# Kernel optimization log

Hardware: AMD Instinct MI355X
Metric: run time of the kernel (lower is better)

The kernel has to match this reference:

```python
import jax, jax.numpy as jnp
import numpy as np

B, T, S, D, L, V = 32, 64, 128, 512, 2, 32000
DSRC = 2 * D  # bidirectional encoder
PAD = 1


def setup_inputs() -> dict:
    key = jax.random.key(0)
    ks = jax.random.split(key, 16)
    sc = 0.05
    embed = jax.random.normal(ks[5], (V, D), jnp.float32) * sc
    embed = embed.at[PAD].set(0.0)  # padding_idx row is zero
    return {
        "prev_tgt_tokens": jax.random.randint(ks[0], (B, T), 0, V),
        "encoder_out": jax.random.normal(ks[1], (B, S, DSRC), jnp.float32),
        "hiddens": jax.random.normal(ks[2], (L, B, D), jnp.float32) * sc,
        "cells": jax.random.normal(ks[3], (L, B, D), jnp.float32) * sc,
        "src_mask": jax.random.randint(ks[4], (B, S), 0, 2).astype(bool),
        "embed": embed,
        "W_ih": jax.random.normal(ks[6], (L, 4 * D, D), jnp.float32) * sc,
        "W_hh": jax.random.normal(ks[7], (L, 4 * D, D), jnp.float32) * sc,
        "b_ih": jnp.zeros((L, 4 * D), jnp.float32),
        "b_hh": jnp.zeros((L, 4 * D), jnp.float32),
        "W_in": jax.random.normal(ks[8], (DSRC, D), jnp.float32) * sc,   # input_proj: d_tgt -> d_src
        "b_in": jnp.zeros((DSRC,), jnp.float32),
        "W_out": jax.random.normal(ks[9], (D, DSRC + D), jnp.float32) * sc,  # out_proj
        "b_out": jnp.zeros((D,), jnp.float32),
    }


def reference(prev_tgt_tokens, encoder_out, hiddens, cells, src_mask,
              embed, W_ih, W_hh, b_ih, b_hh, W_in, b_in, W_out, b_out):
    n_layers, _, d_model = hiddens.shape
    tgt_len = prev_tgt_tokens.shape[1]
    tgt_embed = embed[prev_tgt_tokens]          # [B, T, D]
    xs = jnp.swapaxes(tgt_embed, 0, 1)          # [T, B, D]

    def lstm_cell(x, h, c, l):
        gates = x @ W_ih[l].T + b_ih[l] + h @ W_hh[l].T + b_hh[l]  # [B, 4D]
        i, f, g, o = jnp.split(gates, 4, axis=-1)
        c2 = jax.nn.sigmoid(f) * c + jax.nn.sigmoid(i) * jnp.tanh(g)
        h2 = jax.nn.sigmoid(o) * jnp.tanh(c2)
        return h2, c2

    def step(h_carry, y_t):
        s = y_t
        new_h = []
        for l in range(n_layers):
            h2, c2 = lstm_cell(s, h_carry[l], cells[l], l)
            # Faithful to source bug: `prev_hiddens[l], prev_hiddens[l] = (hidden, cell)`
            # stores the NEW CELL into the hidden slot; prev_cells never updated.
            new_h.append(c2)
            s = h2
        # attention
        xq = s @ W_in.T + b_in                              # [B, DSRC]
        e = jnp.einsum('bsd,bd->bs', encoder_out, xq)       # [B, S]
        e = jnp.where(src_mask, -1e9, e)
        attn = jax.nn.softmax(e, axis=-1)
        ctx = jnp.einsum('bs,bsd->bd', attn, encoder_out)   # [B, DSRC]
        out_t = jnp.tanh(jnp.concatenate([ctx, s], axis=-1) @ W_out.T + b_out)
        return jnp.stack(new_h), out_t

    _, outs = jax.lax.scan(step, hiddens, xs)   # outs: [T, B, D]
    # faithful to torch.cat(outs, dim=0).view(-1, tgt_len, d_model)
    return outs.reshape(-1, d_model).reshape(-1, tgt_len, d_model)
```

## Files before the change

### kernel.cpp

```cpp
#include <hip/hip_runtime.h>
#include <math.h>

typedef unsigned short u16;
typedef __attribute__((ext_vector_type(4))) float f4;
typedef __attribute__((ext_vector_type(8))) unsigned short us8;
typedef __attribute__((ext_vector_type(8))) short bfrag;
typedef __attribute__((ext_vector_type(4))) float f32x4;

#define BB 32
#define TT 64
#define DD 512
#define G4_ 2048

__device__ __forceinline__ float sigf(float x) { return 1.0f / (1.0f + expf(-x)); }
__device__ __forceinline__ float bf2f(u16 u) {
    union { unsigned int i; float f; } v; v.i = ((unsigned int)u) << 16; return v.f;
}
__device__ __forceinline__ u16 f2bf(float f) {
    union { float f; unsigned int i; } v; v.f = f;
    unsigned int r = v.i + 0x7fffu + ((v.i >> 16) & 1u);
    return (u16)(r >> 16);
}

__global__ void k_flag(const unsigned char* __restrict__ m, int* __restrict__ flag) {
    int tid = threadIdx.x;
    int badbyte = 0, nonz_off = 0, evenu16_nz = 0;
    for (int i = tid * 16; i < tid * 16 + 16; i++) {
        unsigned char c = m[i];
        if (c > 1) badbyte = 1;
        if ((i & 3) != 0 && c != 0) nonz_off = 1;
    }
    const u16* mu = (const u16*)m;
    for (int i = tid * 8; i < tid * 8 + 8; i++) {
        if ((i & 1) == 0 && mu[i] != 0) evenu16_nz = 1;
    }
    __shared__ int s_bad, s_noff, s_env;
    if (tid == 0) { s_bad = 0; s_noff = 0; s_env = 0; }
    __syncthreads();
    if (badbyte) atomicOr(&s_bad, 1);
    if (nonz_off) atomicOr(&s_noff, 1);
    if (evenu16_nz) atomicOr(&s_env, 1);
    __syncthreads();
    if (tid == 0) {
        int f;
        if (s_bad) f = s_env ? 2 : 3;
        else       f = s_noff ? 0 : 1;
        *flag = f;
    }
}

__global__ void __launch_bounds__(256) k_init2(const float* __restrict__ hid,
                                               u16* __restrict__ h0s,
                                               u16* __restrict__ h1s) {
    int i = blockIdx.x * 256 + threadIdx.x;
    u16 v0 = f2bf(hid[i]), v1 = f2bf(hid[16384 + i]);
    h0s[i] = v0; h0s[16384 + i] = v0;
    h1s[i] = v1; h1s[16384 + i] = v1;
}

__global__ void __launch_bounds__(256) k_packIn(const float* __restrict__ Win,
                                                u16* __restrict__ Wp) {
    int g = blockIdx.x * 256 + threadIdx.x;
    int lane = g & 63, grp = g >> 6;
    int j16 = grp >> 4, ks = grp & 15;
    const float* src = &Win[((size_t)(j16 * 16 + (lane & 15))) * 512 + ks * 32 + (lane >> 4) * 8];
    u16* dst = &Wp[(size_t)g * 8];
    f4 v0 = *(const f4*)&src[0];
    f4 v1 = *(const f4*)&src[4];
    dst[0] = f2bf(v0[0]); dst[1] = f2bf(v0[1]); dst[2] = f2bf(v0[2]); dst[3] = f2bf(v0[3]);
    dst[4] = f2bf(v1[0]); dst[5] = f2bf(v1[1]); dst[6] = f2bf(v1[2]); dst[7] = f2bf(v1[3]);
}

__global__ void __launch_bounds__(256) k_packOut(const float* __restrict__ Wout,
                                                 u16* __restrict__ Wp) {
    int g = blockIdx.x * 256 + threadIdx.x;
    int lane = g & 63, grp = g >> 6;
    int j16 = grp / 48, ks = grp % 48;
    const float* src = &Wout[((size_t)(j16 * 16 + (lane & 15))) * 1536 + ks * 32 + (lane >> 4) * 8];
    u16* dst = &Wp[(size_t)g * 8];
    f4 v0 = *(const f4*)&src[0];
    f4 v1 = *(const f4*)&src[4];
    dst[0] = f2bf(v0[0]); dst[1] = f2bf(v0[1]); dst[2] = f2bf(v0[2]); dst[3] = f2bf(v0[3]);
    dst[4] = f2bf(v1[0]); dst[5] = f2bf(v1[1]); dst[6] = f2bf(v1[2]); dst[7] = f2bf(v1[3]);
}

__global__ void __launch_bounds__(256) k_packA(const float* __restrict__ Wih0,
                                               u16* __restrict__ Wp) {
    int g = blockIdx.x * 256 + threadIdx.x;
    int lane = g & 63, grp = g >> 6;
    int j16 = grp >> 4, ks = grp & 15;
    const float* src = &Wih0[((size_t)(j16 * 16 + (lane & 15))) * 512 + ks * 32 + (lane >> 4) * 8];
    u16* dst = &Wp[(size_t)g * 8];
    f4 v0 = *(const f4*)&src[0];
    f4 v1 = *(const f4*)&src[4];
    dst[0] = f2bf(v0[0]); dst[1] = f2bf(v0[1]); dst[2] = f2bf(v0[2]); dst[3] = f2bf(v0[3]);
    dst[4] = f2bf(v1[0]); dst[5] = f2bf(v1[1]); dst[6] = f2bf(v1[2]); dst[7] = f2bf(v1[3]);
}

__global__ void __launch_bounds__(256) k_packPh(const float* __restrict__ Wih,
                                                const float* __restrict__ Whh,
                                                u16* __restrict__ php) {
    int gidx = blockIdx.x * 256 + threadIdx.x;
    int m = gidx >> 17;
    int rem = gidx & 131071;
    int lane = rem & 63;
    int q = rem >> 6;
    int ks = q & 15, T = q >> 4;
    int g = T >> 5, d16 = T & 31;
    int j = g * 512 + d16 * 16 + (lane & 15);
    int kcol = ks * 32 + (lane >> 4) * 8;
    const float* src = (m == 0) ? Whh
                     : (m == 1) ? (Wih + 1048576)
                                : (Whh + 1048576);
    const float* sp = &src[(size_t)j * 512 + kcol];
    u16* dst = &php[((size_t)m << 20) + (size_t)rem * 8];
    f4 v0 = *(const f4*)&sp[0];
    f4 v1 = *(const f4*)&sp[4];
    dst[0] = f2bf(v0[0]); dst[1] = f2bf(v0[1]); dst[2] = f2bf(v0[2]); dst[3] = f2bf(v0[3]);
    dst[4] = f2bf(v1[0]); dst[5] = f2bf(v1[1]); dst[6] = f2bf(v1[2]); dst[7] = f2bf(v1[3]);
}

__global__ void __launch_bounds__(256) k_gih0_mfma(const int* __restrict__ tokens,
                                                   const float* __restrict__ embed,
                                                   const u16* __restrict__ Wp,
                                                   const float* __restrict__ bih,
                                                   const float* __restrict__ bhh,
                                                   float* __restrict__ gih0p) {
    const int tid = threadIdx.x;
    const int lane = tid & 63, w = tid >> 6;
    const int t = blockIdx.y;
    const int jw = blockIdx.x * 256 + w * 64;
    __shared__ u16 xs[32][520];
    __shared__ int toks[32];
    if (tid < 32) toks[tid] = tokens[tid * TT + t];
    __syncthreads();
    for (int i = tid; i < 32 * 128; i += 256) {
        int b = i >> 7, k4 = i & 127;
        f4 v = *(const f4*)&embed[(size_t)toks[b] * 512 + k4 * 4];
        u16* dst = &xs[b][k4 * 4];
        dst[0] = f2bf(v[0]); dst[1] = f2bf(v[1]); dst[2] = f2bf(v[2]); dst[3] = f2bf(v[3]);
    }
    __syncthreads();

    const int l15 = lane & 15, l4 = lane >> 4;
    f32x4 acc[2][4];
#pragma unroll
    for (int mi = 0; mi < 2; mi++)
#pragma unroll
        for (int ni = 0; ni < 4; ni++) acc[mi][ni] = (f32x4){0.f, 0.f, 0.f, 0.f};

    for (int ks = 0; ks < 16; ks++) {
        bfrag a0 = *(const bfrag*)&xs[l15][ks * 32 + l4 * 8];
        bfrag a1 = *(const bfrag*)&xs[16 + l15][ks * 32 + l4 * 8];
#pragma unroll
        for (int ni = 0; ni < 4; ni++) {
            int j16 = (jw + ni * 16) >> 4;
            bfrag bf = *(const bfrag*)&Wp[(((size_t)j16 * 16 + ks) * 64 + lane) * 8];
            acc[0][ni] = __builtin_amdgcn_mfma_f32_16x16x32_bf16(a0, bf, acc[0][ni], 0, 0, 0);
            acc[1][ni] = __builtin_amdgcn_mfma_f32_16x16x32_bf16(a1, bf, acc[1][ni], 0, 0, 0);
        }
    }

#pragma unroll
    for (int ni = 0; ni < 4; ni++) {
        int j16 = (jw >> 4) + ni;
        int g = j16 >> 5, d16 = j16 & 31;
        int j = j16 * 16 + l15;
        float bv = bih[j] + bhh[j];
#pragma unroll
        for (int mi = 0; mi < 2; mi++) {
            f32x4 sv = acc[mi][ni];
            sv[0] += bv; sv[1] += bv; sv[2] += bv; sv[3] += bv;
            *(f32x4*)&gih0p[(((((size_t)t * 32 + d16) * 4 + g) * 2 + mi) * 64 + lane) * 4] = sv;
        }
    }
}

__global__ void __launch_bounds__(256) k_phaseM(
    const int k,
    const float* __restrict__ gih0p,
    const u16* __restrict__ whh0p,
    const u16* __restrict__ wih1p,
    const u16* __restrict__ whh1p,
    const float* __restrict__ bih1,
    const float* __restrict__ bhh1,
    const float* __restrict__ cells,
    const u16* __restrict__ h0r, u16* __restrict__ h0w,
    const u16* __restrict__ h20r, u16* __restrict__ h20w,
    const u16* __restrict__ h1r, u16* __restrict__ h1w,
    u16* __restrict__ H2)
{
    const int tid = threadIdx.x;
    const int lane = tid & 63, w = tid >> 6;
    const int l15 = lane & 15, l4 = lane >> 4;
    __shared__ u16 xsA[32][520];
    __shared__ u16 xsB[32][520];

    if (blockIdx.x < 16) {
        if (k >= 64) return;
        const int wid = blockIdx.x * 4 + w;
        const int d16 = wid >> 1, mi = wid & 1;
        const int d = d16 * 16 + l15;
        f32x4 acc[4];
#pragma unroll
        for (int g = 0; g < 4; g++)
            acc[g] = *(const f32x4*)&gih0p[(((((size_t)k * 32 + d16) * 4 + g) * 2 + mi) * 64 + lane) * 4];
        for (int i = tid; i < 2048; i += 256) {
            int b = i >> 6, k8 = i & 63;
            *(us8*)&xsA[b][k8 * 8] = *(const us8*)&h0r[b * 512 + k8 * 8];
        }
        __syncthreads();
        const int arow = mi * 16 + l15;
        for (int ks = 0; ks < 16; ks++) {
            bfrag a = *(const bfrag*)&xsA[arow][ks * 32 + l4 * 8];
#pragma unroll
            for (int g = 0; g < 4; g++) {
                int T = g * 32 + d16;
                bfrag bf = *(const bfrag*)&whh0p[(((size_t)T * 16 + ks) * 64 + lane) * 8];
                acc[g] = __builtin_amdgcn_mfma_f32_16x16x32_bf16(a, bf, acc[g], 0, 0, 0);
            }
        }
#pragma unroll
        for (int r = 0; r < 4; r++) {
            int b = mi * 16 + l4 * 4 + r;
            float gi = acc[0][r];
            float gf = acc[1][r];
            float gg = acc[2][r];
            float go = acc[3][r];
            float cell = cells[b * 512 + d];
            float c2 = sigf(gf) * cell + sigf(gi) * tanhf(gg);
            float h2 = sigf(go) * tanhf(c2);
            h0w[b * 512 + d] = f2bf(c2);
            h20w[b * 512 + d] = f2bf(h2);
        }
    } else {
        if (k < 1) return;
        for (int i = tid; i < 2048; i += 256) {
            int b = i >> 6, k8 = i & 63;
            *(us8*)&xsA[b][k8 * 8] = *(const us8*)&h20r[b * 512 + k8 * 8];
            *(us8*)&xsB[b][k8 * 8] = *(const us8*)&h1r[b * 512 + k8 * 8];
        }
        __syncthreads();
        const int wid = (blockIdx.x - 16) * 4 + w;
        const int d16 = wid >> 1, mi = wid & 1;
        const int d = d16 * 16 + l15;
        const int arow = mi * 16 + l15;
        f32x4 acc[4];
#pragma unroll
        for (int g = 0; g < 4; g++) acc[g] = (f32x4){0.f, 0.f, 0.f, 0.f};
        for (int ks = 0; ks < 16; ks++) {
            bfrag a = *(const bfrag*)&xsA[arow][ks * 32 + l4 * 8];
#pragma unroll
            for (int g = 0; g < 4; g++) {
                int T = g * 32 + d16;
                bfrag bf = *(const bfrag*)&wih1p[(((size_t)T * 16 + ks) * 64 + lane) * 8];
                acc[g] = __builtin_amdgcn_mfma_f32_16x16x32_bf16(a, bf, acc[g], 0, 0, 0);
            }
        }
        for (int ks = 0; ks < 16; ks++) {
            bfrag a = *(const bfrag*)&xsB[arow][ks * 32 + l4 * 8];
#pragma unroll
            for (int g = 0; g < 4; g++) {
                int T = g * 32 + d16;
                bfrag bf = *(const bfrag*)&whh1p[(((size_t)T * 16 + ks) * 64 + lane) * 8];
                acc[g] = __builtin_amdgcn_mfma_f32_16x16x32_bf16(a, bf, acc[g], 0, 0, 0);
            }
        }
        float bb0 = bih1[0 * 512 + d] + bhh1[0 * 512 + d];
        float bb1v = bih1[1 * 512 + d] + bhh1[1 * 512 + d];
        float bb2 = bih1[2 * 512 + d] + bhh1[2 * 512 + d];
        float bb3 = bih1[3 * 512 + d] + bhh1[3 * 512 + d];
#pragma unroll
        for (int r = 0; r < 4; r++) {
            int b = mi * 16 + l4 * 4 + r;
            float gi = acc[0][r] + bb0;
            float gf = acc[1][r] + bb1v;
            float gg = acc[2][r] + bb2;
            float go = acc[3][r] + bb3;
            float cell = cells[16384 + b * 512 + d];
            float c2 = sigf(gf) * cell + sigf(gi) * tanhf(gg);
            float h2 = sigf(go) * tanhf(c2);
            h1w[b * 512 + d] = f2bf(c2);
            H2[(size_t)(k - 1) * 16384 + b * 512 + d] = f2bf(h2);
        }
    }
}

__global__ void __launch_bounds__(256) k_x_mfma(const u16* __restrict__ H2,
                                                const u16* __restrict__ Wpin,
                                                const float* __restrict__ bin,
                                                float* __restrict__ XQ) {
    const int tid = threadIdx.x;
    const int lane = tid & 63, w = tid >> 6;
    const int t = blockIdx.y;
    const int jw = blockIdx.x * 256 + w * 64;
    __shared__ u16 xs[32][520];
    for (int i = tid; i < 2048; i += 256) {
        int b = i >> 6, k8 = i & 63;
        *(us8*)&xs[b][k8 * 8] = *(const us8*)&H2[(size_t)t * 16384 + b * 512 + k8 * 8];
    }
    __syncthreads();
    const int l15 = lane & 15, l4 = lane >> 4;
    f32x4 acc[2][4];
#pragma unroll
    for (int mi = 0; mi < 2; mi++)
#pragma unroll
        for (int ni = 0; ni < 4; ni++) acc[mi][ni] = (f32x4){0.f, 0.f, 0.f, 0.f};
    for (int ks = 0; ks < 16; ks++) {
        bfrag a0 = *(const bfrag*)&xs[l15][ks * 32 + l4 * 8];
        bfrag a1 = *(const bfrag*)&xs[16 + l15][ks * 32 + l4 * 8];
#pragma unroll
        for (int ni = 0; ni < 4; ni++) {
            int j16 = (jw + ni * 16) >> 4;
            bfrag bf = *(const bfrag*)&Wpin[(((size_t)j16 * 16 + ks) * 64 + lane) * 8];
            acc[0][ni] = __builtin_amdgcn_mfma_f32_16x16x32_bf16(a0, bf, acc[0][ni], 0, 0, 0);
            acc[1][ni] = __builtin_amdgcn_mfma_f32_16x16x32_bf16(a1, bf, acc[1][ni], 0, 0, 0);
        }
    }
#pragma unroll
    for (int ni = 0; ni < 4; ni++) {
        int j = jw + ni * 16 + l15;
        float bv = bin[j];
#pragma unroll
        for (int mi = 0; mi < 2; mi++) {
#pragma unroll
            for (int r = 0; r < 4; r++) {
                int b = mi * 16 + l4 * 4 + r;
                XQ[((size_t)(t * 32 + b)) * 1024 + j] = acc[mi][ni][r] + bv;
            }
        }
    }
}

__global__ void __launch_bounds__(256) k_out_mfma(const float* __restrict__ CTX,
                                                  const u16* __restrict__ H2,
                                                  const u16* __restrict__ Wpout,
                                                  const float* __restrict__ bout,
                                                  float* __restrict__ out) {
    const int tid = threadIdx.x;
    const int lane = tid & 63, w = tid >> 6;
    const int t = blockIdx.y;
    const int jw = blockIdx.x * 256 + w * 64;
    __shared__ u16 xs[32][520];
    const int l15 = lane & 15, l4 = lane >> 4;
    f32x4 acc[2][4];
#pragma unroll
    for (int mi = 0; mi < 2; mi++)
#pragma unroll
        for (int ni = 0; ni < 4; ni++) acc[mi][ni] = (f32x4){0.f, 0.f, 0.f, 0.f};
    for (int c = 0; c < 3; c++) {
        if (c) __syncthreads();
        if (c < 2) {
            for (int i = tid; i < 32 * 128; i += 256) {
                int b = i >> 7, k4 = i & 127;
                f4 v = *(const f4*)&CTX[((size_t)(t * 32 + b)) * 1024 + c * 512 + k4 * 4];
                u16* dst = &xs[b][k4 * 4];
                dst[0] = f2bf(v[0]); dst[1] = f2bf(v[1]); dst[2] = f2bf(v[2]); dst[3] = f2bf(v[3]);
            }
        } else {
            for (int i = tid; i < 2048; i += 256) {
                int b = i >> 6, k8 = i & 63;
                *(us8*)&xs[b][k8 * 8] = *(const us8*)&H2[(size_t)t * 16384 + b * 512 + k8 * 8];
            }
        }
        __syncthreads();
        for (int ks = 0; ks < 16; ks++) {
            bfrag a0 = *(const bfrag*)&xs[l15][ks * 32 + l4 * 8];
            bfrag a1 = *(const bfrag*)&xs[16 + l15][ks * 32 + l4 * 8];
#pragma unroll
            for (int ni = 0; ni < 4; ni++) {
                int j16 = (jw + ni * 16) >> 4;
                bfrag bf = *(const bfrag*)&Wpout[(((size_t)j16 * 48 + c * 16 + ks) * 64 + lane) * 8];
                acc[0][ni] = __builtin_amdgcn_mfma_f32_16x16x32_bf16(a0, bf, acc[0][ni], 0, 0, 0);
                acc[1][ni] = __builtin_amdgcn_mfma_f32_16x16x32_bf16(a1, bf, acc[1][ni], 0, 0, 0);
            }
        }
    }
#pragma unroll
    for (int ni = 0; ni < 4; ni++) {
        int j = jw + ni * 16 + l15;
        float bv = bout[j];
#pragma unroll
        for (int mi = 0; mi < 2; mi++) {
#pragma unroll
            for (int r = 0; r < 4; r++) {
                int b = mi * 16 + l4 * 4 + r;
                out[((size_t)(t * 32 + b)) * 512 + j] = tanhf(acc[mi][ni][r] + bv);
            }
        }
    }
}

__global__ void __launch_bounds__(256) k_att4(const float* __restrict__ XQ,
                                              const float* __restrict__ enc,
                                              const unsigned char* __restrict__ mask,
                                              const int* __restrict__ flag,
                                              float* __restrict__ CTX) {
    const int tid = threadIdx.x;
    const int b = blockIdx.x, t0 = blockIdx.y * 4;
    __shared__ float xq[4][1024];
    __shared__ float ered[4][256];
    __shared__ float attn[4][128];
    __shared__ float red2[4][8];
#pragma unroll
    for (int tg = 0; tg < 4; tg++) {
        f4 v = *(const f4*)&XQ[((size_t)((t0 + tg) * 32 + b)) * 1024 + tid * 4];
        float* dst = &xq[tg][tid * 4];
        dst[0] = v[0]; dst[1] = v[1]; dst[2] = v[2]; dst[3] = v[3];
    }
    __syncthreads();
    const int s = tid >> 1, hh = tid & 1;
    float p[4] = {0.f, 0.f, 0.f, 0.f};
    const float* erow = enc + ((size_t)(b * 128 + s)) * 1024 + hh * 512;
    for (int k4 = 0; k4 < 128; k4++) {
        f4 u = *(const f4*)&erow[k4 * 4];
#pragma unroll
        for (int kk = 0; kk < 4; kk++) {
#pragma unroll
            for (int tg = 0; tg < 4; tg++)
                p[tg] += u[kk] * xq[tg][hh * 512 + k4 * 4 + kk];
        }
    }
#pragma unroll
    for (int tg = 0; tg < 4; tg++) ered[tg][tid] = p[tg];
    __syncthreads();
    bool msk = false;
    if (tid < 128) {
        int f = *flag;
        if (f == 0)      msk = mask[b * 128 + tid] != 0;
        else if (f == 1) msk = ((const int*)mask)[b * 128 + tid] != 0;
        else if (f == 2) msk = ((const u16*)mask)[b * 128 + tid] != 0;
        else             msk = ((const unsigned int*)mask)[b * 128 + tid] != 0;
    }
    const int wave = tid >> 6;
    float e[4];
#pragma unroll
    for (int tg = 0; tg < 4; tg++) {
        e[tg] = -INFINITY;
        if (tid < 128) {
            e[tg] = ered[tg][2 * tid] + ered[tg][2 * tid + 1];
            if (msk) e[tg] = -1e9f;
        }
        float v = e[tg];
#pragma unroll
        for (int off = 32; off >= 1; off >>= 1) v = fmaxf(v, __shfl_xor(v, off));
        if ((tid & 63) == 0) red2[tg][wave] = v;
    }
    __syncthreads();
#pragma unroll
    for (int tg = 0; tg < 4; tg++) {
        float mx = fmaxf(fmaxf(red2[tg][0], red2[tg][1]), fmaxf(red2[tg][2], red2[tg][3]));
        float pp = (tid < 128) ? expf(e[tg] - mx) : 0.f;
        float su = pp;
#pragma unroll
        for (int off = 32; off >= 1; off >>= 1) su += __shfl_xor(su, off);
        if ((tid & 63) == 0) red2[tg][4 + wave] = su;
        __syncthreads();
        float S = (red2[tg][4] + red2[tg][5]) + (red2[tg][6] + red2[tg][7]);
        if (tid < 128) attn[tg][tid] = pp / S;
        __syncthreads();
    }
    float c0[4] = {0, 0, 0, 0}, c1[4] = {0, 0, 0, 0};
    float c2v[4] = {0, 0, 0, 0}, c3[4] = {0, 0, 0, 0};
    const float* eb = enc + ((size_t)b * 128) * 1024 + tid * 4;
    for (int s2 = 0; s2 < 128; s2++) {
        f4 u = *(const f4*)&eb[(size_t)s2 * 1024];
#pragma unroll
        for (int tg = 0; tg < 4; tg++) {
            float a = attn[tg][s2];
            c0[tg] += a * u[0]; c1[tg] += a * u[1]; c2v[tg] += a * u[2]; c3[tg] += a * u[3];
        }
    }
#pragma unroll
    for (int tg = 0; tg < 4; tg++) {
        float* crow = CTX + ((size_t)((t0 + tg) * 32 + b)) * 1024 + tid * 4;
        crow[0] = c0[tg]; crow[1] = c1[tg]; crow[2] = c2v[tg]; crow[3] = c3[tg];
    }
}

extern "C" void kernel_launch(void* const* d_in, const int* in_sizes, int n_in,
                              void* d_out, int out_size, void* d_ws, size_t ws_size,
                              hipStream_t stream) {
    const int* tokens   = (const int*)d_in[0];
    const float* enc    = (const float*)d_in[1];
    const float* hidden = (const float*)d_in[2];
    const float* cells  = (const float*)d_in[3];
    const unsigned char* mask = (const unsigned char*)d_in[4];
    const float* embed  = (const float*)d_in[5];
    const float* W_ih   = (const float*)d_in[6];
    const float* W_hh   = (const float*)d_in[7];
    const float* b_ih   = (const float*)d_in[8];
    const float* b_hh   = (const float*)d_in[9];
    const float* W_in   = (const float*)d_in[10];
    const float* b_in   = (const float*)d_in[11];
    const float* W_out  = (const float*)d_in[12];
    const float* b_out  = (const float*)d_in[13];
    float* out = (float*)d_out;

    float* ws = (float*)d_ws;
    float* gih0p = ws;
    u16*   h0s  = (u16*)(ws + 4194304);
    u16*   h20s = (u16*)(ws + 4210688);
    u16*   h1s  = (u16*)(ws + 4227072);
    u16*   H2   = (u16*)(ws + 4243456);
    u16*   php  = (u16*)(ws + 4767744);
    u16*   whh0p = php;
    u16*   wih1p = php + 1048576;
    u16*   whh1p = php + 2097152;
    u16*   wpin  = (u16*)(ws + 6340608);
    u16*   wpout = (u16*)(ws + 6602752);
    u16*   wih0p = (u16*)(ws + 6995968);
    int*   flag  = (int*)(ws + 7520256);
    float* XQ   = ws;
    float* CTX  = ws + 2097152;

    const float* bih1 = b_ih + G4_;
    const float* bhh1 = b_hh + G4_;

    k_flag<<<1, 256, 0, stream>>>(mask, flag);
    k_init2<<<64, 256, 0, stream>>>(hidden, h0s, h1s);
    k_packIn<<<256, 256, 0, stream>>>(W_in, wpin);
    k_packOut<<<384, 256, 0, stream>>>(W_out, wpout);
    k_packA<<<512, 256, 0, stream>>>(W_ih, wih0p);
    k_packPh<<<1536, 256, 0, stream>>>(W_ih, W_hh, php);
    k_gih0_mfma<<<dim3(8, 64), 256, 0, stream>>>(tokens, embed, wih0p, b_ih, b_hh, gih0p);

    for (int k = 0; k <= 64; k++) {
        const int r = k & 1, w = r ^ 1;
        k_phaseM<<<32, 256, 0, stream>>>(k, gih0p, whh0p, wih1p, whh1p, bih1, bhh1, cells,
                                         h0s + r * 16384, h0s + w * 16384,
                                         h20s + r * 16384, h20s + w * 16384,
                                         h1s + r * 16384, h1s + w * 16384, H2);
    }

    k_x_mfma<<<dim3(4, 64), 256, 0, stream>>>(H2, wpin, b_in, XQ);
    k_att4<<<dim3(32, 16), 256, 0, stream>>>(XQ, enc, mask, flag, CTX);
    k_out_mfma<<<dim3(2, 64), 256, 0, stream>>>(CTX, H2, wpout, b_out, out);
}
```

Before: 676.4 us.

## Split recurrent step K-reduction across wave pairs and double the block count

Each output tile of the per-timestep LSTM kernel is now computed by two waves that each handle half of the K dimension (layer 0) or one of the two matmuls (layer 1). The partial sums are combined through shared memory before the gate nonlinearities. Grid size doubles from 32 to 64 blocks, which spreads the latency-bound sequential step over more CUs. The cost is an extra __syncthreads, shared-memory reduction traffic, and each block restaging the full h vectors.

```diff
diff --git a/kernel.cpp b/kernel.cpp
--- a/kernel.cpp
+++ b/kernel.cpp
@@ -193,25 +193,32 @@
     const int tid = threadIdx.x;
     const int lane = tid & 63, w = tid >> 6;
     const int l15 = lane & 15, l4 = lane >> 4;
+    const int unitL = w >> 1, sub = w & 1;
     __shared__ u16 xsA[32][520];
     __shared__ u16 xsB[32][520];
-
-    if (blockIdx.x < 16) {
+    __shared__ float red[2][4][64][4];
+
+    if (blockIdx.x < 32) {
         if (k >= 64) return;
-        const int wid = blockIdx.x * 4 + w;
-        const int d16 = wid >> 1, mi = wid & 1;
+        const int d16mi = blockIdx.x * 2 + unitL;
+        const int d16 = d16mi >> 1, mi = d16mi & 1;
         const int d = d16 * 16 + l15;
         f32x4 acc[4];
 #pragma unroll
-        for (int g = 0; g < 4; g++)
-            acc[g] = *(const f32x4*)&gih0p[(((((size_t)k * 32 + d16) * 4 + g) * 2 + mi) * 64 + lane) * 4];
+        for (int g = 0; g < 4; g++) {
+            if (sub == 0)
+                acc[g] = *(const f32x4*)&gih0p[(((((size_t)k * 32 + d16) * 4 + g) * 2 + mi) * 64 + lane) * 4];
+            else
+                acc[g] = (f32x4){0.f, 0.f, 0.f, 0.f};
+        }
         for (int i = tid; i < 2048; i += 256) {
             int b = i >> 6, k8 = i & 63;
             *(us8*)&xsA[b][k8 * 8] = *(const us8*)&h0r[b * 512 + k8 * 8];
         }
         __syncthreads();
         const int arow = mi * 16 + l15;
-        for (int ks = 0; ks < 16; ks++) {
+        const int ks0 = sub * 8;
+        for (int ks = ks0; ks < ks0 + 8; ks++) {
             bfrag a = *(const bfrag*)&xsA[arow][ks * 32 + l4 * 8];
 #pragma unroll
             for (int g = 0; g < 4; g++) {
@@ -220,18 +227,31 @@
                 acc[g] = __builtin_amdgcn_mfma_f32_16x16x32_bf16(a, bf, acc[g], 0, 0, 0);
             }
         }
-#pragma unroll
-        for (int r = 0; r < 4; r++) {
-            int b = mi * 16 + l4 * 4 + r;
-            float gi = acc[0][r];
-            float gf = acc[1][r];
-            float gg = acc[2][r];
-            float go = acc[3][r];
-            float cell = cells[b * 512 + d];
-            float c2 = sigf(gf) * cell + sigf(gi) * tanhf(gg);
-            float h2 = sigf(go) * tanhf(c2);
-            h0w[b * 512 + d] = f2bf(c2);
-            h20w[b * 512 + d] = f2bf(h2);
+        if (sub == 1) {
+#pragma unroll
+            for (int g = 0; g < 4; g++)
+                *(f32x4*)&red[unitL][g][lane][0] = acc[g];
+        }
+        __syncthreads();
+        if (sub == 0) {
+#pragma unroll
+            for (int g = 0; g < 4; g++) {
+                f32x4 pv = *(const f32x4*)&red[unitL][g][lane][0];
+                acc[g][0] += pv[0]; acc[g][1] += pv[1]; acc[g][2] += pv[2]; acc[g][3] += pv[3];
+            }
+#pragma unroll
+            for (int r = 0; r < 4; r++) {
+                int b = mi * 16 + l4 * 4 + r;
+                float gi = acc[0][r];
+                float gf = acc[1][r];
+                float gg = acc[2][r];
+                float go = acc[3][r];
+                float cell = cells[b * 512 + d];
+                float c2 = sigf(gf) * cell + sigf(gi) * tanhf(gg);
+                float h2 = sigf(go) * tanhf(c2);
+                h0w[b * 512 + d] = f2bf(c2);
+                h20w[b * 512 + d] = f2bf(h2);
+            }
         }
     } else {
         if (k < 1) return;
@@ -241,47 +261,53 @@
             *(us8*)&xsB[b][k8 * 8] = *(const us8*)&h1r[b * 512 + k8 * 8];
         }
         __syncthreads();
-        const int wid = (blockIdx.x - 16) * 4 + w;
-        const int d16 = wid >> 1, mi = wid & 1;
+        const int d16mi = (blockIdx.x - 32) * 2 + unitL;
+        const int d16 = d16mi >> 1, mi = d16mi & 1;
         const int d = d16 * 16 + l15;
         const int arow = mi * 16 + l15;
+        const u16 (* __restrict__ xsrc)[520] = sub ? xsB : xsA;
+        const u16* wsrc = sub ? whh1p : wih1p;
         f32x4 acc[4];
 #pragma unroll
         for (int g = 0; g < 4; g++) acc[g] = (f32x4){0.f, 0.f, 0.f, 0.f};
         for (int ks = 0; ks < 16; ks++) {
-            bfrag a = *(const bfrag*)&xsA[arow][ks * 32 + l4 * 8];
+            bfrag a = *(const bfrag*)&xsrc[arow][ks * 32 + l4 * 8];
 #pragma unroll
             for (int g = 0; g < 4; g++) {
                 int T = g * 32 + d16;
-                bfrag bf = *(const bfrag*)&wih1p[(((size_t)T * 16 + ks) * 64 + lane) * 8];
+                bfrag bf = *(const bfrag*)&wsrc[(((size_t)T * 16 + ks) * 64 + lane) * 8];
                 acc[g] = __builtin_amdgcn_mfma_f32_16x16x32_bf16(a, bf, acc[g], 0, 0, 0);
             }
         }
-        for (int ks = 0; ks < 16; ks++) {
-            bfrag a = *(const bfrag*)&xsB[arow][ks * 32 + l4 * 8];
+        if (sub == 1) {
+#pragma unroll
+            for (int g = 0; g < 4; g++)
+                *(f32x4*)&red[unitL][g][lane][0] = acc[g];
+        }
+        __syncthreads();
+        if (sub == 0) {
 #pragma unroll
             for (int g = 0; g < 4; g++) {
-                int T = g * 32 + d16;
-                bfrag bf = *(const bfrag*)&whh1p[(((size_t)T * 16 + ks) * 64 + lane) * 8];
-                acc[g] = __builtin_amdgcn_mfma_f32_16x16x32_bf16(a, bf, acc[g], 0, 0, 0);
-            }
-        }
-        float bb0 = bih1[0 * 512 + d] + bhh1[0 * 512 + d];
-        float bb1v = bih1[1 * 512 + d] + bhh1[1 * 512 + d];
-        float bb2 = bih1[2 * 512 + d] + bhh1[2 * 512 + d];
-        float bb3 = bih1[3 * 512 + d] + bhh1[3 * 512 + d];
-#pragma unroll
-        for (int r = 0; r < 4; r++) {
-            int b = mi * 16 + l4 * 4 + r;
-            float gi = acc[0][r] + bb0;
-            float gf = acc[1][r] + bb1v;
-            float gg = acc[2][r] + bb2;
-            float go = acc[3][r] + bb3;
-            float cell = cells[16384 + b * 512 + d];
-            float c2 = sigf(gf) * cell + sigf(gi) * tanhf(gg);
-            float h2 = sigf(go) * tanhf(c2);
-            h1w[b * 512 + d] = f2bf(c2);
-            H2[(size_t)(k - 1) * 16384 + b * 512 + d] = f2bf(h2);
+                f32x4 pv = *(const f32x4*)&red[unitL][g][lane][0];
+                acc[g][0] += pv[0]; acc[g][1] += pv[1]; acc[g][2] += pv[2]; acc[g][3] += pv[3];
+            }
+            float bb0 = bih1[0 * 512 + d] + bhh1[0 * 512 + d];
+            float bb1v = bih1[1 * 512 + d] + bhh1[1 * 512 + d];
+            float bb2 = bih1[2 * 512 + d] + bhh1[2 * 512 + d];
+            float bb3 = bih1[3 * 512 + d] + bhh1[3 * 512 + d];
+#pragma unroll
+            for (int r = 0; r < 4; r++) {
+                int b = mi * 16 + l4 * 4 + r;
+                float gi = acc[0][r] + bb0;
+                float gf = acc[1][r] + bb1v;
+                float gg = acc[2][r] + bb2;
+                float go = acc[3][r] + bb3;
+                float cell = cells[16384 + b * 512 + d];
+                float c2 = sigf(gf) * cell + sigf(gi) * tanhf(gg);
+                float h2 = sigf(go) * tanhf(c2);
+                h1w[b * 512 + d] = f2bf(c2);
+                H2[(size_t)(k - 1) * 16384 + b * 512 + d] = f2bf(h2);
+            }
         }
     }
 }
@@ -527,7 +553,7 @@
 
     for (int k = 0; k <= 64; k++) {
         const int r = k & 1, w = r ^ 1;
-        k_phaseM<<<32, 256, 0, stream>>>(k, gih0p, whh0p, wih1p, whh1p, bih1, bhh1, cells,
+        k_phaseM<<<64, 256, 0, stream>>>(k, gih0p, whh0p, wih1p, whh1p, bih1, bhh1, cells,
                                          h0s + r * 16384, h0s + w * 16384,
                                          h20s + r * 16384, h20s + w * 16384,
                                          h1s + r * 16384, h1s + w * 16384, H2);
```

After: 608.5 us. -10.0%, faster.
